# Kernel tuning notes

Measured on AMD Instinct MI355X. Metric: run time of the kernel, lower is better.

The kernel has to match this reference:

```python
import jax, jax.numpy as jnp
import numpy as np

HIDDEN = 1024

def setup_inputs() -> dict:
    key = jax.random.key(0)
    k1, k2, k3, k4, k5 = jax.random.split(key, 5)
    B, T, E2, H = 32, 2048, 1024, HIDDEN
    scale = 1.0 / np.sqrt(H)
    x = jax.random.normal(k1, (B, T, E2), dtype=jnp.float32)
    W_ih = jax.random.uniform(k2, (4 * H, E2), minval=-scale, maxval=scale, dtype=jnp.float32)
    W_hh = jax.random.uniform(k3, (4 * H, H), minval=-scale, maxval=scale, dtype=jnp.float32)
    b_ih = jax.random.uniform(k4, (4 * H,), minval=-scale, maxval=scale, dtype=jnp.float32)
    b_hh = jax.random.uniform(k5, (4 * H,), minval=-scale, maxval=scale, dtype=jnp.float32)
    return {"x": x, "W_ih": W_ih, "W_hh": W_hh, "b_ih": b_ih, "b_hh": b_hh}

def reference(x, W_ih, W_hh, b_ih, b_hh):
    B, T, _ = x.shape
    H = W_hh.shape[1]
    # Precompute input contribution for all timesteps: [T, B, 4H]
    x_proj = jnp.einsum('bte,ge->tbg', x, W_ih) + b_ih + b_hh

    def step(carry, xp_t):
        h, c = carry
        gates = xp_t + h @ W_hh.T  # [B, 4H]
        i, f, g, o = jnp.split(gates, 4, axis=-1)  # torch gate order i,f,g,o
        i = jax.nn.sigmoid(i)
        f = jax.nn.sigmoid(f)
        g = jnp.tanh(g)
        o = jax.nn.sigmoid(o)
        c_new = f * c + i * g
        h_new = o * jnp.tanh(c_new)
        return (h_new, c_new), None

    h0 = jnp.zeros((B, H), dtype=x.dtype)
    c0 = jnp.zeros((B, H), dtype=x.dtype)
    (h_t, c_t), _ = jax.lax.scan(step, (h0, c0), x_proj)
    return (h_t, c_t)
```

## Files before the change

### kernel.cpp

```cpp
#include <hip/hip_runtime.h>
#include <stdint.h>

#define T_STEPS 2048
#define HID 1024
#define G4 4096
#define NWG 64

typedef __attribute__((ext_vector_type(8))) short short8;
typedef __attribute__((ext_vector_type(4))) float float4v;
typedef __attribute__((ext_vector_type(4))) unsigned int uint4v;
typedef unsigned long long ull;

#define HBUF_OFF 0ull
#define FLAG_OFF 131072ull
#define DT_OFF   132608ull
#define CST_OFF  135168ull
#define XP_OFF   0x100000ull

__device__ inline unsigned short f2bf(float f) {
  union { float f; unsigned int u; } v; v.f = f;
  unsigned int u = v.u;
  return (unsigned short)((u + 0x7fffu + ((u >> 16) & 1u)) >> 16);
}
__device__ inline float bf2f(unsigned short h) {
  union { unsigned int u; float f; } v; v.u = ((unsigned int)h) << 16;
  return v.f;
}
__device__ inline short8 pack8(float4 a, float4 b) {
  short8 r;
  r[0] = (short)f2bf(a.x); r[1] = (short)f2bf(a.y);
  r[2] = (short)f2bf(a.z); r[3] = (short)f2bf(a.w);
  r[4] = (short)f2bf(b.x); r[5] = (short)f2bf(b.y);
  r[6] = (short)f2bf(b.z); r[7] = (short)f2bf(b.w);
  return r;
}

__global__ void dtype_sniff(const unsigned short* __restrict__ w,
                            unsigned int* __restrict__ dt) {
  __shared__ int red[256];
  const int tid = threadIdx.x;
  int cnt = 0;
#pragma unroll
  for (int i = 0; i < 4; i++) {
    unsigned short h = w[tid * 4 + i];
    unsigned e = (h >> 7) & 0xFF;
    if (h == 0 || (e >= 100 && e <= 123)) cnt++;
  }
  red[tid] = cnt;
  __syncthreads();
  for (int s = 128; s > 0; s >>= 1) {
    if (tid < s) red[tid] += red[tid + s];
    __syncthreads();
  }
  if (tid == 0) dt[0] = (red[0] >= 922) ? 1u : 0u;
}

__global__ __launch_bounds__(256) void xproj_gemm(
    const void* __restrict__ x, const void* __restrict__ Wih,
    const void* __restrict__ bih, const void* __restrict__ bhh,
    unsigned short* __restrict__ xp, int t0,
    const unsigned int* __restrict__ dt)
{
  __shared__ char smem[32768];
  __shared__ float bias_s[128];
  unsigned short* As = (unsigned short*)smem;
  unsigned short* Bs = (unsigned short*)(smem + 10240);

  const bool isbf = (*dt != 0);

  const int bid = blockIdx.x;
  const int panel = bid >> 9;
  const int within = bid & 511;
  const int nt = within & 31;
  const int mt = (panel << 4) + (within >> 5);
  const int m0 = mt * 128;
  const int n0 = nt * 128;
  const int tl0 = m0 >> 5;

  const int tid = threadIdx.x;
  if (tid < 128) {
    bias_s[tid] = isbf
        ? bf2f(((const unsigned short*)bih)[n0 + tid]) +
          bf2f(((const unsigned short*)bhh)[n0 + tid])
        : ((const float*)bih)[n0 + tid] + ((const float*)bhh)[n0 + tid];
  }

  const int w = tid >> 6, lane = tid & 63;
  const int quad = lane >> 4, lr = lane & 15;
  const int wm = (w & 1) * 64, wn = (w >> 1) * 64;

  float4v acc[4][4];
#pragma unroll
  for (int i = 0; i < 4; i++)
#pragma unroll
    for (int j = 0; j < 4; j++) acc[i][j] = (float4v){0.f, 0.f, 0.f, 0.f};

  const int r = tid >> 1, half = tid & 1;
  const size_t aoff =
      ((size_t)(r & 31) * T_STEPS + (size_t)(t0 + tl0 + (r >> 5))) * HID + half * 16;
  const size_t boff = (size_t)(n0 + r) * HID + half * 16;
  unsigned short* adst = As + r * 40 + half * 16;
  unsigned short* bdst = Bs + r * 40 + half * 16;

  for (int k0 = 0; k0 < HID; k0 += 32) {
    __syncthreads();
    if (isbf) {
      const unsigned short* a16 = (const unsigned short*)x + aoff + k0;
      const unsigned short* b16 = (const unsigned short*)Wih + boff + k0;
      *(short8*)(adst)     = *(const short8*)(a16);
      *(short8*)(adst + 8) = *(const short8*)(a16 + 8);
      *(short8*)(bdst)     = *(const short8*)(b16);
      *(short8*)(bdst + 8) = *(const short8*)(b16 + 8);
    } else {
      const float4* af = (const float4*)((const float*)x + aoff + k0);
      const float4* bf = (const float4*)((const float*)Wih + boff + k0);
      float4 a0 = af[0], a1 = af[1], a2 = af[2], a3 = af[3];
      float4 b0 = bf[0], b1 = bf[1], b2 = bf[2], b3 = bf[3];
      *(short8*)(adst)     = pack8(a0, a1);
      *(short8*)(adst + 8) = pack8(a2, a3);
      *(short8*)(bdst)     = pack8(b0, b1);
      *(short8*)(bdst + 8) = pack8(b2, b3);
    }
    __syncthreads();
    short8 afr[4], bfr[4];
#pragma unroll
    for (int i = 0; i < 4; i++)
      afr[i] = *(const short8*)(As + (wm + i * 16 + lr) * 40 + quad * 8);
#pragma unroll
    for (int j = 0; j < 4; j++)
      bfr[j] = *(const short8*)(Bs + (wn + j * 16 + lr) * 40 + quad * 8);
#pragma unroll
    for (int i = 0; i < 4; i++)
#pragma unroll
      for (int j = 0; j < 4; j++)
        acc[i][j] = __builtin_amdgcn_mfma_f32_16x16x32_bf16(afr[i], bfr[j], acc[i][j], 0, 0, 0);
  }

  __syncthreads();
  unsigned short* ep = (unsigned short*)smem;
#pragma unroll
  for (int i = 0; i < 4; i++)
#pragma unroll
    for (int j = 0; j < 4; j++)
#pragma unroll
      for (int rr = 0; rr < 4; rr++) {
        int ml = wm + i * 16 + quad * 4 + rr;
        int nl = wn + j * 16 + lr;
        float v = acc[i][j][rr] + bias_s[nl];
        ep[(((ml >> 5) * 128) + nl) * 32 + (ml & 31)] = f2bf(v);
      }
  __syncthreads();
#pragma unroll
  for (int tl = 0; tl < 4; tl++) {
    const uint4* s4 = (const uint4*)(smem + tl * 8192);
    uint4* d4 = (uint4*)(xp + ((size_t)(tl0 + tl) * G4 + n0) * 32);
    for (int i = tid; i < 512; i += 256) d4[i] = s4[i];
  }
}

__global__ __launch_bounds__(256, 1) void lstm_rec(
    const void* __restrict__ Whh,
    const unsigned short* __restrict__ xp,
    unsigned short* __restrict__ hbuf,
    unsigned int* __restrict__ flags,
    float* __restrict__ cstate,
    void* __restrict__ out,
    int t0, int tc,
    const unsigned int* __restrict__ dt)
{
  __shared__ float gpart[4][64][36];

  const bool isbf = (*dt != 0);
  const int wg = blockIdx.x;
  const int tid = threadIdx.x;
  const int w = tid >> 6, lane = tid & 63;
  const int quad = lane >> 4, lr = lane & 15;

  short8 bfrag[32];
#pragma unroll
  for (int q = 0; q < 4; q++) {
    const size_t grow = (size_t)q * HID + wg * 16 + lr;
    if (isbf) {
      const unsigned short* wrow = (const unsigned short*)Whh + grow * HID;
#pragma unroll
      for (int s = 0; s < 8; s++)
        bfrag[q * 8 + s] = *(const short8*)(wrow + w * 256 + s * 32 + quad * 8);
    } else {
      const float* wrow = (const float*)Whh + grow * HID;
#pragma unroll
      for (int s = 0; s < 8; s++) {
        float4 f0 = *(const float4*)(wrow + w * 256 + s * 32 + quad * 8);
        float4 f1 = *(const float4*)(wrow + w * 256 + s * 32 + quad * 8 + 4);
        bfrag[q * 8 + s] = pack8(f0, f1);
      }
    }
  }

  const int cb = 8 * w + (lane >> 3);
  const int ck = lane & 7;
  const int j0 = 2 * ck, j1 = j0 + 1;
  const int gc0 = wg * 16 + j0, gc1 = gc0 + 1;
  float cs0 = cstate[(size_t)cb * HID + gc0];
  float cs1 = cstate[(size_t)cb * HID + gc1];
  long budget = 50000000;

  const int gbase_off = w * 16384 + (quad >> 1) * 1024 + lr * 32 + (quad & 1) * 16;

  for (int t = t0; t < t0 + tc; t++) {
    const unsigned short* xpt = xp + (size_t)(t - t0) * (G4 * 32);
    unsigned short rx0 = xpt[(size_t)gc0 * 32 + cb];
    unsigned short rx1 = xpt[(size_t)(HID + gc0) * 32 + cb];
    unsigned short rx2 = xpt[(size_t)(2 * HID + gc0) * 32 + cb];
    unsigned short rx3 = xpt[(size_t)(3 * HID + gc0) * 32 + cb];
    unsigned short rx4 = xpt[(size_t)gc1 * 32 + cb];
    unsigned short rx5 = xpt[(size_t)(HID + gc1) * 32 + cb];
    unsigned short rx6 = xpt[(size_t)(2 * HID + gc1) * 32 + cb];
    unsigned short rx7 = xpt[(size_t)(3 * HID + gc1) * 32 + cb];

    {
      const unsigned target = (unsigned)t;
      const unsigned int* fp = flags + 64 * w + lane;
      while (__hip_atomic_load(fp, __ATOMIC_RELAXED, __HIP_MEMORY_SCOPE_AGENT) < target) {
        if (--budget < 0) break;
        __builtin_amdgcn_s_sleep(1);
      }
    }

    short8 av[2][8];
    {
      const char* gb = (const char*)hbuf + (size_t)(t & 1) * 65536 + gbase_off;
#define GL(m, s) \
      asm volatile("global_load_dwordx4 %0, %1, off sc0 sc1" \
                   : "=v"(av[m][s]) : "v"(gb + (s) * 2048 + (m) * 512) : "memory")
      GL(0, 0); GL(1, 0); GL(0, 1); GL(1, 1);
      GL(0, 2); GL(1, 2); GL(0, 3); GL(1, 3);
      GL(0, 4); GL(1, 4); GL(0, 5); GL(1, 5);
      GL(0, 6); GL(1, 6); GL(0, 7); GL(1, 7);
#undef GL
      asm volatile("s_waitcnt vmcnt(0)" ::: "memory");
      __builtin_amdgcn_sched_barrier(0);
    }

    float4v acc[2][4];
#pragma unroll
    for (int m = 0; m < 2; m++)
#pragma unroll
      for (int q = 0; q < 4; q++) acc[m][q] = (float4v){0.f, 0.f, 0.f, 0.f};
#pragma unroll
    for (int s = 0; s < 8; s++) {
#pragma unroll
      for (int q = 0; q < 4; q++) {
        acc[0][q] = __builtin_amdgcn_mfma_f32_16x16x32_bf16(av[0][s], bfrag[q * 8 + s], acc[0][q], 0, 0, 0);
        acc[1][q] = __builtin_amdgcn_mfma_f32_16x16x32_bf16(av[1][s], bfrag[q * 8 + s], acc[1][q], 0, 0, 0);
      }
    }

    __syncthreads();
#pragma unroll
    for (int m = 0; m < 2; m++)
#pragma unroll
      for (int q = 0; q < 4; q++)
        *(float4v*)&gpart[w][q * 16 + lr][m * 16 + quad * 4] = acc[m][q];
    __syncthreads();

    {
      float gi0 = bf2f(rx0), gf0 = bf2f(rx1), gg0 = bf2f(rx2), go0 = bf2f(rx3);
      float gi1 = bf2f(rx4), gf1 = bf2f(rx5), gg1 = bf2f(rx6), go1 = bf2f(rx7);
#pragma unroll
      for (int p = 0; p < 4; p++) {
        gi0 += gpart[p][j0][cb];
        gf0 += gpart[p][16 + j0][cb];
        gg0 += gpart[p][32 + j0][cb];
        go0 += gpart[p][48 + j0][cb];
        gi1 += gpart[p][j1][cb];
        gf1 += gpart[p][16 + j1][cb];
        gg1 += gpart[p][32 + j1][cb];
        go1 += gpart[p][48 + j1][cb];
      }
      float si0 = 1.f / (1.f + __expf(-gi0));
      float sf0 = 1.f / (1.f + __expf(-gf0));
      float tg0 = tanhf(gg0);
      float so0 = 1.f / (1.f + __expf(-go0));
      cs0 = sf0 * cs0 + si0 * tg0;
      float hn0 = so0 * tanhf(cs0);

      float si1 = 1.f / (1.f + __expf(-gi1));
      float sf1 = 1.f / (1.f + __expf(-gf1));
      float tg1 = tanhf(gg1);
      float so1 = 1.f / (1.f + __expf(-go1));
      cs1 = sf1 * cs1 + si1 * tg1;
      float hn1 = so1 * tanhf(cs1);

      unsigned pk = (unsigned)f2bf(hn0) | ((unsigned)f2bf(hn1) << 16);
      unsigned int* hb32 = (unsigned int*)hbuf;
      const unsigned idx = (unsigned)(((t + 1) & 1) * 16384 + wg * 256 + cb * 8 + ck);
      __hip_atomic_store(hb32 + idx, pk, __ATOMIC_RELAXED, __HIP_MEMORY_SCOPE_AGENT);

      if (t == T_STEPS - 1) {
        if (isbf) {
          unsigned short* ob = (unsigned short*)out;
          ob[(size_t)cb * HID + gc0] = f2bf(hn0);
          ob[(size_t)cb * HID + gc1] = f2bf(hn1);
          ob[32768 + (size_t)cb * HID + gc0] = f2bf(cs0);
          ob[32768 + (size_t)cb * HID + gc1] = f2bf(cs1);
        } else {
          float* of = (float*)out;
          of[(size_t)cb * HID + gc0] = hn0;
          of[(size_t)cb * HID + gc1] = hn1;
          of[32768 + (size_t)cb * HID + gc0] = cs0;
          of[32768 + (size_t)cb * HID + gc1] = cs1;
        }
      }
    }
    asm volatile("s_waitcnt vmcnt(0)" ::: "memory");
    if (lane == 0)
      __hip_atomic_store(&flags[wg * 4 + w], (unsigned)(t + 1), __ATOMIC_RELAXED,
                         __HIP_MEMORY_SCOPE_AGENT);
  }

  cstate[(size_t)cb * HID + gc0] = cs0;
  cstate[(size_t)cb * HID + gc1] = cs1;
}

extern "C" void kernel_launch(void* const* d_in, const int* in_sizes, int n_in,
                              void* d_out, int out_size, void* d_ws, size_t ws_size,
                              hipStream_t stream) {
  (void)in_sizes; (void)n_in; (void)out_size;
  const void* x   = d_in[0];
  const void* Wih = d_in[1];
  const void* Whh = d_in[2];
  const void* bih = d_in[3];
  const void* bhh = d_in[4];

  char* ws = (char*)d_ws;
  unsigned short* hbuf   = (unsigned short*)(ws + HBUF_OFF);
  unsigned int*   flags  = (unsigned int*)(ws + FLAG_OFF);
  unsigned int*   dt     = (unsigned int*)(ws + DT_OFF);
  float*          cstate = (float*)(ws + CST_OFF);
  unsigned short* xp     = (unsigned short*)(ws + XP_OFF);

  int tc = 2048;
  while (tc > 16 && XP_OFF + (size_t)tc * 262144ull > ws_size) tc >>= 1;

  hipMemsetAsync(ws, 0, CST_OFF + 131072, stream);

  hipLaunchKernelGGL(dtype_sniff, dim3(1), dim3(256), 0, stream,
                     (const unsigned short*)Wih, dt);

  for (int t0 = 0; t0 < T_STEPS; t0 += tc) {
    hipLaunchKernelGGL(xproj_gemm, dim3(tc * 8), dim3(256), 0, stream,
                       x, Wih, bih, bhh, xp, t0, dt);
    hipLaunchKernelGGL(lstm_rec, dim3(NWG), dim3(256), 0, stream,
                       Whh, xp, hbuf, flags, cstate, d_out, t0, tc, dt);
  }
}
```

Before: 11.12 ms.

## Replace flag-based step sync with timestep-tagged hidden-state words

Each hidden-state word is stored as a 64-bit value that carries the bf16 pair plus the timestep tag. Consumers poll by loading the h buffer directly until every tag matches, which removes the separate flag poll, the vmcnt wait before signalling, and the flag store. The LDS partial-sum buffer is double-buffered by step parity so one __syncthreads per step can be dropped. In exchange each load of the h data is twice as large, the spin loop reissues full vector loads, and correctness depends on 64-bit stores being seen atomically.

```diff
diff --git a/kernel.cpp b/kernel.cpp
--- a/kernel.cpp
+++ b/kernel.cpp
@@ -12,9 +12,8 @@
 typedef unsigned long long ull;
 
 #define HBUF_OFF 0ull
-#define FLAG_OFF 131072ull
-#define DT_OFF   132608ull
-#define CST_OFF  135168ull
+#define DT_OFF   262144ull
+#define CST_OFF  266240ull
 #define XP_OFF   0x100000ull
 
 __device__ inline unsigned short f2bf(float f) {
@@ -161,14 +160,13 @@
 __global__ __launch_bounds__(256, 1) void lstm_rec(
     const void* __restrict__ Whh,
     const unsigned short* __restrict__ xp,
-    unsigned short* __restrict__ hbuf,
-    unsigned int* __restrict__ flags,
+    ull* __restrict__ hbuf,
     float* __restrict__ cstate,
     void* __restrict__ out,
     int t0, int tc,
     const unsigned int* __restrict__ dt)
 {
-  __shared__ float gpart[4][64][36];
+  __shared__ float gpart[2][4][64][36];
 
   const bool isbf = (*dt != 0);
   const int wg = blockIdx.x;
@@ -202,9 +200,9 @@
   const int gc0 = wg * 16 + j0, gc1 = gc0 + 1;
   float cs0 = cstate[(size_t)cb * HID + gc0];
   float cs1 = cstate[(size_t)cb * HID + gc1];
-  long budget = 50000000;
-
-  const int gbase_off = w * 16384 + (quad >> 1) * 1024 + lr * 32 + (quad & 1) * 16;
+  long budget = 200000000;
+
+  const int goff = (16 * w + (quad >> 1)) * 2048 + lr * 64 + (quad & 1) * 32;
 
   for (int t = t0; t < t0 + tc; t++) {
     const unsigned short* xpt = xp + (size_t)(t - t0) * (G4 * 32);
@@ -217,28 +215,35 @@
     unsigned short rx6 = xpt[(size_t)(2 * HID + gc1) * 32 + cb];
     unsigned short rx7 = xpt[(size_t)(3 * HID + gc1) * 32 + cb];
 
+    uint4v lb[32];
     {
-      const unsigned target = (unsigned)t;
-      const unsigned int* fp = flags + 64 * w + lane;
-      while (__hip_atomic_load(fp, __ATOMIC_RELAXED, __HIP_MEMORY_SCOPE_AGENT) < target) {
+      const char* gb = (const char*)hbuf + (size_t)(t & 1) * 131072 + goff;
+      const unsigned tagt = (unsigned)t;
+      for (;;) {
+#pragma unroll
+        for (int s = 0; s < 8; s++) {
+          const char* p = gb + s * 4096;
+          asm volatile(
+              "global_load_dwordx4 %0, %4, off sc0 sc1\n\t"
+              "global_load_dwordx4 %1, %4, off offset:16 sc0 sc1\n\t"
+              "global_load_dwordx4 %2, %4, off offset:1024 sc0 sc1\n\t"
+              "global_load_dwordx4 %3, %4, off offset:1040 sc0 sc1"
+              : "=v"(lb[4 * s]), "=v"(lb[4 * s + 1]),
+                "=v"(lb[4 * s + 2]), "=v"(lb[4 * s + 3])
+              : "v"(p) : "memory");
+        }
+        asm volatile("s_waitcnt vmcnt(0)" ::: "memory");
+        __builtin_amdgcn_sched_barrier(0);
+        unsigned mn = 0xFFFFFFFFu;
+#pragma unroll
+        for (int i = 0; i < 32; i++) {
+          unsigned ta = lb[i][1], tb = lb[i][3];
+          unsigned mi = ta < tb ? ta : tb;
+          mn = mi < mn ? mi : mn;
+        }
+        if (__all(mn == tagt)) break;
         if (--budget < 0) break;
-        __builtin_amdgcn_s_sleep(1);
-      }
-    }
-
-    short8 av[2][8];
-    {
-      const char* gb = (const char*)hbuf + (size_t)(t & 1) * 65536 + gbase_off;
-#define GL(m, s) \
-      asm volatile("global_load_dwordx4 %0, %1, off sc0 sc1" \
-                   : "=v"(av[m][s]) : "v"(gb + (s) * 2048 + (m) * 512) : "memory")
-      GL(0, 0); GL(1, 0); GL(0, 1); GL(1, 1);
-      GL(0, 2); GL(1, 2); GL(0, 3); GL(1, 3);
-      GL(0, 4); GL(1, 4); GL(0, 5); GL(1, 5);
-      GL(0, 6); GL(1, 6); GL(0, 7); GL(1, 7);
-#undef GL
-      asm volatile("s_waitcnt vmcnt(0)" ::: "memory");
-      __builtin_amdgcn_sched_barrier(0);
+      }
     }
 
     float4v acc[2][4];
@@ -248,19 +253,26 @@
       for (int q = 0; q < 4; q++) acc[m][q] = (float4v){0.f, 0.f, 0.f, 0.f};
 #pragma unroll
     for (int s = 0; s < 8; s++) {
+      uint4v pa, pb;
+      pa[0] = lb[4 * s][0];     pa[1] = lb[4 * s][2];
+      pa[2] = lb[4 * s + 1][0]; pa[3] = lb[4 * s + 1][2];
+      pb[0] = lb[4 * s + 2][0]; pb[1] = lb[4 * s + 2][2];
+      pb[2] = lb[4 * s + 3][0]; pb[3] = lb[4 * s + 3][2];
+      short8 a0 = *(short8*)&pa;
+      short8 a1 = *(short8*)&pb;
 #pragma unroll
       for (int q = 0; q < 4; q++) {
-        acc[0][q] = __builtin_amdgcn_mfma_f32_16x16x32_bf16(av[0][s], bfrag[q * 8 + s], acc[0][q], 0, 0, 0);
-        acc[1][q] = __builtin_amdgcn_mfma_f32_16x16x32_bf16(av[1][s], bfrag[q * 8 + s], acc[1][q], 0, 0, 0);
-      }
-    }
-
-    __syncthreads();
+        acc[0][q] = __builtin_amdgcn_mfma_f32_16x16x32_bf16(a0, bfrag[q * 8 + s], acc[0][q], 0, 0, 0);
+        acc[1][q] = __builtin_amdgcn_mfma_f32_16x16x32_bf16(a1, bfrag[q * 8 + s], acc[1][q], 0, 0, 0);
+      }
+    }
+
+    const int pp = t & 1;
 #pragma unroll
     for (int m = 0; m < 2; m++)
 #pragma unroll
       for (int q = 0; q < 4; q++)
-        *(float4v*)&gpart[w][q * 16 + lr][m * 16 + quad * 4] = acc[m][q];
+        *(float4v*)&gpart[pp][w][q * 16 + lr][m * 16 + quad * 4] = acc[m][q];
     __syncthreads();
 
     {
@@ -268,14 +280,14 @@
       float gi1 = bf2f(rx4), gf1 = bf2f(rx5), gg1 = bf2f(rx6), go1 = bf2f(rx7);
 #pragma unroll
       for (int p = 0; p < 4; p++) {
-        gi0 += gpart[p][j0][cb];
-        gf0 += gpart[p][16 + j0][cb];
-        gg0 += gpart[p][32 + j0][cb];
-        go0 += gpart[p][48 + j0][cb];
-        gi1 += gpart[p][j1][cb];
-        gf1 += gpart[p][16 + j1][cb];
-        gg1 += gpart[p][32 + j1][cb];
-        go1 += gpart[p][48 + j1][cb];
+        gi0 += gpart[pp][p][j0][cb];
+        gf0 += gpart[pp][p][16 + j0][cb];
+        gg0 += gpart[pp][p][32 + j0][cb];
+        go0 += gpart[pp][p][48 + j0][cb];
+        gi1 += gpart[pp][p][j1][cb];
+        gf1 += gpart[pp][p][16 + j1][cb];
+        gg1 += gpart[pp][p][32 + j1][cb];
+        go1 += gpart[pp][p][48 + j1][cb];
       }
       float si0 = 1.f / (1.f + __expf(-gi0));
       float sf0 = 1.f / (1.f + __expf(-gf0));
@@ -292,9 +304,9 @@
       float hn1 = so1 * tanhf(cs1);
 
       unsigned pk = (unsigned)f2bf(hn0) | ((unsigned)f2bf(hn1) << 16);
-      unsigned int* hb32 = (unsigned int*)hbuf;
-      const unsigned idx = (unsigned)(((t + 1) & 1) * 16384 + wg * 256 + cb * 8 + ck);
-      __hip_atomic_store(hb32 + idx, pk, __ATOMIC_RELAXED, __HIP_MEMORY_SCOPE_AGENT);
+      ull pv = (ull)pk | ((ull)(unsigned)(t + 1) << 32);
+      ull* dst = hbuf + (size_t)((t + 1) & 1) * 16384 + wg * 256 + cb * 8 + ck;
+      __hip_atomic_store(dst, pv, __ATOMIC_RELAXED, __HIP_MEMORY_SCOPE_AGENT);
 
       if (t == T_STEPS - 1) {
         if (isbf) {
@@ -312,10 +324,6 @@
         }
       }
     }
-    asm volatile("s_waitcnt vmcnt(0)" ::: "memory");
-    if (lane == 0)
-      __hip_atomic_store(&flags[wg * 4 + w], (unsigned)(t + 1), __ATOMIC_RELAXED,
-                         __HIP_MEMORY_SCOPE_AGENT);
   }
 
   cstate[(size_t)cb * HID + gc0] = cs0;
@@ -333,11 +341,10 @@
   const void* bhh = d_in[4];
 
   char* ws = (char*)d_ws;
-  unsigned short* hbuf   = (unsigned short*)(ws + HBUF_OFF);
-  unsigned int*   flags  = (unsigned int*)(ws + FLAG_OFF);
-  unsigned int*   dt     = (unsigned int*)(ws + DT_OFF);
-  float*          cstate = (float*)(ws + CST_OFF);
-  unsigned short* xp     = (unsigned short*)(ws + XP_OFF);
+  ull*          hbuf   = (ull*)(ws + HBUF_OFF);
+  unsigned int* dt     = (unsigned int*)(ws + DT_OFF);
+  float*        cstate = (float*)(ws + CST_OFF);
+  unsigned short* xp   = (unsigned short*)(ws + XP_OFF);
 
   int tc = 2048;
   while (tc > 16 && XP_OFF + (size_t)tc * 262144ull > ws_size) tc >>= 1;
@@ -351,6 +358,6 @@
     hipLaunchKernelGGL(xproj_gemm, dim3(tc * 8), dim3(256), 0, stream,
                        x, Wih, bih, bhh, xp, t0, dt);
     hipLaunchKernelGGL(lstm_rec, dim3(NWG), dim3(256), 0, stream,
-                       Whh, xp, hbuf, flags, cstate, d_out, t0, tc, dt);
-  }
-}
+                       Whh, xp, hbuf, cstate, d_out, t0, tc, dt);
+  }
+}
```

New measurement: 11.29 ms. Within noise of the previous version (+1.6%).
